# Optimization experiments

Hardware: AMD Instinct MI355X
Metric: run time of the kernel (lower is better)

Reference implementation:

```python
import jax, jax.numpy as jnp
import numpy as np

BETA = 1.0
JITTER = 1e-6


def setup_inputs() -> dict:
    key = jax.random.key(0)
    k1, k2, k3, k4 = jax.random.split(key, 4)
    N, L = 256, 8192
    R_clean = jax.random.normal(k1, (N, L, 3, 3), dtype=jnp.float32)
    t = jax.random.uniform(k2, (N,), dtype=jnp.float32, minval=0.05, maxval=1.0)
    noise = jax.random.normal(k3, (N, L, 3, 3), dtype=jnp.float32)
    eps_noise = jax.random.normal(k4, (N, L, 3, 3), dtype=jnp.float32)
    return {"R_clean": R_clean, "t": t, "noise": noise, "eps_noise": eps_noise}


def _svd_project_so3(F):
    # F: (..., 3, 3).  R = U diag(1,1,det(U V^T)) V^T
    U, S, Vh = jnp.linalg.svd(F, full_matrices=False)
    d = jnp.linalg.det(jnp.matmul(U, Vh))          # (...,)
    mid = jnp.concatenate(
        [jnp.ones(d.shape + (2,), dtype=F.dtype), d[..., None]], axis=-1
    )                                               # (..., 3) = (1, 1, det)
    # U @ diag(mid) @ Vh == (U * mid[..., None, :]) @ Vh
    return jnp.matmul(U * mid[..., None, :], Vh)


def reference(R_clean, t, noise, eps_noise):
    # sample_theta: F_t = alpha_t * R_clean + sqrt(alpha_t) * noise
    alpha_t = (BETA * t).reshape(-1, 1, 1, 1)       # (N,1,1,1)
    F_t = alpha_t * R_clean + jnp.sqrt(alpha_t) * noise
    # svd_project_so3 adds a tiny random jitter before SVD
    F = F_t + JITTER * eps_noise
    return _svd_project_so3(F)
```

## Files before the change

### kernel.cpp

```cpp
#include <hip/hip_runtime.h>

#define TPB  256
#define MPB  256
#define F4PB 576

__device__ __forceinline__ void jrot(float app, float aqq, float apq,
                                     float& c, float& s, float& t) {
    float d  = aqq - app;
    float p2 = apq + apq;
    float rad = __builtin_amdgcn_sqrtf(fmaf(d, d, p2 * p2));
    float den = fmaxf(fabsf(d) + rad, 1e-38f);
    t = p2 * copysignf(__builtin_amdgcn_rcpf(den), d);
    c = __builtin_amdgcn_rsqf(fmaf(t, t, 1.0f));
    s = t * c;
}

__global__ __launch_bounds__(TPB)
void so3_proj_kernel(const float* __restrict__ Rc,
                     const float* __restrict__ Tt,
                     const float* __restrict__ Nz,
                     const float* __restrict__ Ez,
                     float* __restrict__ Out,
                     int L)
{
    __shared__ float4 lds4[F4PB];
    float* lds = (float*)lds4;

    const int tid = threadIdx.x;
    const long long base = (long long)blockIdx.x * MPB;
    const int n = (int)(base / (long long)L);
    const float alpha = Tt[n];
    const float sa = __builtin_amdgcn_sqrtf(alpha);

    const float4* R4 = (const float4*)(Rc + base * 9);
    const float4* N4 = (const float4*)(Nz + base * 9);
    const float4* E4 = (const float4*)(Ez + base * 9);
    float4*       O4 = (float4*)(Out + base * 9);

    #pragma unroll
    for (int it = 0; it < 3; ++it) {
        int j = tid + it * TPB;
        if (j < F4PB) {
            float4 r = R4[j], z = N4[j], e = E4[j];
            float4 f;
            f.x = fmaf(alpha, r.x, fmaf(sa, z.x, 1e-6f * e.x));
            f.y = fmaf(alpha, r.y, fmaf(sa, z.y, 1e-6f * e.y));
            f.z = fmaf(alpha, r.z, fmaf(sa, z.z, 1e-6f * e.z));
            f.w = fmaf(alpha, r.w, fmaf(sa, z.w, 1e-6f * e.w));
            lds4[j] = f;
        }
    }
    __syncthreads();

    float F[9];
    #pragma unroll
    for (int k = 0; k < 9; ++k) F[k] = lds[tid * 9 + k];

    float a00 = F[0]*F[0] + F[3]*F[3] + F[6]*F[6];
    float a01 = F[0]*F[1] + F[3]*F[4] + F[6]*F[7];
    float a02 = F[0]*F[2] + F[3]*F[5] + F[6]*F[8];
    float a11 = F[1]*F[1] + F[4]*F[4] + F[7]*F[7];
    float a12 = F[1]*F[2] + F[4]*F[5] + F[7]*F[8];
    float a22 = F[2]*F[2] + F[5]*F[5] + F[8]*F[8];

    float v00=1.f, v01=0.f, v02=0.f;
    float v10=0.f, v11=1.f, v12=0.f;
    float v20=0.f, v21=0.f, v22=1.f;

    for (int sweep = 0; sweep < 5; ++sweep) {
        if (sweep >= 3) {
            float off = fmaf(a01, a01, fmaf(a02, a02, a12 * a12));
            float sc  = fmaf(a00, a00, fmaf(a11, a11, a22 * a22));
            if (__all(off <= 1e-13f * sc)) break;
        }
        float c, s, t, t0;
        jrot(a00, a11, a01, c, s, t);
        a00 = fmaf(-t, a01, a00); a11 = fmaf(t, a01, a11); a01 = 0.f;
        t0 = c*a02 - s*a12; a12 = fmaf(s, a02, c*a12); a02 = t0;
        t0 = c*v00 - s*v01; v01 = fmaf(s, v00, c*v01); v00 = t0;
        t0 = c*v10 - s*v11; v11 = fmaf(s, v10, c*v11); v10 = t0;
        t0 = c*v20 - s*v21; v21 = fmaf(s, v20, c*v21); v20 = t0;
        jrot(a00, a22, a02, c, s, t);
        a00 = fmaf(-t, a02, a00); a22 = fmaf(t, a02, a22); a02 = 0.f;
        t0 = c*a01 - s*a12; a12 = fmaf(s, a01, c*a12); a01 = t0;
        t0 = c*v00 - s*v02; v02 = fmaf(s, v00, c*v02); v00 = t0;
        t0 = c*v10 - s*v12; v12 = fmaf(s, v10, c*v12); v10 = t0;
        t0 = c*v20 - s*v22; v22 = fmaf(s, v20, c*v22); v20 = t0;
        jrot(a11, a22, a12, c, s, t);
        a11 = fmaf(-t, a12, a11); a22 = fmaf(t, a12, a22); a12 = 0.f;
        t0 = c*a01 - s*a02; a02 = fmaf(s, a01, c*a02); a01 = t0;
        t0 = c*v01 - s*v02; v02 = fmaf(s, v01, c*v02); v01 = t0;
        t0 = c*v11 - s*v12; v12 = fmaf(s, v11, c*v12); v11 = t0;
        t0 = c*v21 - s*v22; v22 = fmaf(s, v21, c*v22); v21 = t0;
    }

    float l0 = a00, l1 = a11, l2 = a22;
    if (l0 < l1) { float t;
        t=l0;l0=l1;l1=t; t=v00;v00=v01;v01=t; t=v10;v10=v11;v11=t; t=v20;v20=v21;v21=t; }
    if (l0 < l2) { float t;
        t=l0;l0=l2;l2=t; t=v00;v00=v02;v02=t; t=v10;v10=v12;v12=t; t=v20;v20=v22;v22=t; }
    if (l1 < l2) { float t;
        t=l1;l1=l2;l2=t; t=v01;v01=v02;v02=t; t=v11;v11=v12;v12=t; t=v21;v21=v22;v22=t; }

    float v3x = v10*v21 - v20*v11;
    float v3y = v20*v01 - v00*v21;
    float v3z = v00*v11 - v10*v01;

    float u1x = F[0]*v00 + F[1]*v10 + F[2]*v20;
    float u1y = F[3]*v00 + F[4]*v10 + F[5]*v20;
    float u1z = F[6]*v00 + F[7]*v10 + F[8]*v20;
    float inv1 = __builtin_amdgcn_rsqf(fmaxf(u1x*u1x + u1y*u1y + u1z*u1z, 1e-30f));
    u1x *= inv1; u1y *= inv1; u1z *= inv1;

    float wx = F[0]*v01 + F[1]*v11 + F[2]*v21;
    float wy = F[3]*v01 + F[4]*v11 + F[5]*v21;
    float wz = F[6]*v01 + F[7]*v11 + F[8]*v21;
    float dd = u1x*wx + u1y*wy + u1z*wz;
    wx -= dd*u1x; wy -= dd*u1y; wz -= dd*u1z;
    float inv2 = __builtin_amdgcn_rsqf(fmaxf(wx*wx + wy*wy + wz*wz, 1e-30f));
    float u2x = wx*inv2, u2y = wy*inv2, u2z = wz*inv2;

    float u3x = u1y*u2z - u1z*u2y;
    float u3y = u1z*u2x - u1x*u2z;
    float u3z = u1x*u2y - u1y*u2x;

    float Rm[9];
    Rm[0] = u1x*v00 + u2x*v01 + u3x*v3x;
    Rm[1] = u1x*v10 + u2x*v11 + u3x*v3y;
    Rm[2] = u1x*v20 + u2x*v21 + u3x*v3z;
    Rm[3] = u1y*v00 + u2y*v01 + u3y*v3x;
    Rm[4] = u1y*v10 + u2y*v11 + u3y*v3y;
    Rm[5] = u1y*v20 + u2y*v21 + u3y*v3z;
    Rm[6] = u1z*v00 + u2z*v01 + u3z*v3x;
    Rm[7] = u1z*v10 + u2z*v11 + u3z*v3y;
    Rm[8] = u1z*v20 + u2z*v21 + u3z*v3z;

    __syncthreads();
    #pragma unroll
    for (int k = 0; k < 9; ++k) lds[tid * 9 + k] = Rm[k];
    __syncthreads();

    #pragma unroll
    for (int it = 0; it < 3; ++it) {
        int j = tid + it * TPB;
        if (j < F4PB) O4[j] = lds4[j];
    }
}

extern "C" void kernel_launch(void* const* d_in, const int* in_sizes, int n_in,
                              void* d_out, int out_size, void* d_ws, size_t ws_size,
                              hipStream_t stream) {
    const float* Rc = (const float*)d_in[0];
    const float* Tt = (const float*)d_in[1];
    const float* Nz = (const float*)d_in[2];
    const float* Ez = (const float*)d_in[3];
    float* Out = (float*)d_out;

    const long long mats = (long long)in_sizes[0] / 9;
    const int L = (int)(mats / in_sizes[1]);
    const int blocks = (int)(mats / MPB);

    so3_proj_kernel<<<blocks, TPB, 0, stream>>>(Rc, Tt, Nz, Ez, Out, L);
}
```

Measured before the change: 244.3 us.

## Process two matrices per thread and use closed-form Jacobi rotation updates

Each thread now handles two 3x3 matrices, with the Jacobi pivots of the two interleaved so their independent dependency chains can overlap, and each block covers 512 matrices. The rotation is rewritten so the diagonal entries are updated in closed form, (sum ± rad)/2, and c and s come from a single rsq instead of rcp followed by rsq. The intent is more instruction-level parallelism in the latency-bound Jacobi loop and a shorter per-pivot dependency chain. In exchange, register pressure and LDS use double (18 KB per block), which may reduce occupancy, and the early-exit check now waits for both matrices to converge.

```diff
diff --git a/kernel.cpp b/kernel.cpp
--- a/kernel.cpp
+++ b/kernel.cpp
@@ -1,18 +1,77 @@
 #include <hip/hip_runtime.h>
 
 #define TPB  256
-#define MPB  256
-#define F4PB 576
+#define MPB  512
+#define F4PB 1152
 
-__device__ __forceinline__ void jrot(float app, float aqq, float apq,
-                                     float& c, float& s, float& t) {
-    float d  = aqq - app;
-    float p2 = apq + apq;
+__device__ __forceinline__ void pivot(float& app, float& aqq, float& apq,
+                                      float& arp, float& arq,
+                                      float& vp0, float& vq0,
+                                      float& vp1, float& vq1,
+                                      float& vp2, float& vq2)
+{
+    float d   = aqq - app;
+    float p2  = apq + apq;
     float rad = __builtin_amdgcn_sqrtf(fmaf(d, d, p2 * p2));
-    float den = fmaxf(fabsf(d) + rad, 1e-38f);
-    t = p2 * copysignf(__builtin_amdgcn_rcpf(den), d);
-    c = __builtin_amdgcn_rsqf(fmaf(t, t, 1.0f));
-    s = t * c;
+    float h   = fabsf(d) + rad + 1e-18f;
+    float inv = __builtin_amdgcn_rsqf(fmaf(h, h, p2 * p2));
+    float c   = h * inv;
+    float s   = p2 * copysignf(inv, d);
+    float sum = app + aqq;
+    float sr  = copysignf(rad, d);
+    app = 0.5f * (sum - sr);
+    aqq = 0.5f * (sum + sr);
+    apq = 0.f;
+    float x;
+    x = fmaf(c, arp, -s * arq); arq = fmaf(s, arp, c * arq); arp = x;
+    x = fmaf(c, vp0, -s * vq0); vq0 = fmaf(s, vp0, c * vq0); vp0 = x;
+    x = fmaf(c, vp1, -s * vq1); vq1 = fmaf(s, vp1, c * vq1); vp1 = x;
+    x = fmaf(c, vp2, -s * vq2); vq2 = fmaf(s, vp2, c * vq2); vp2 = x;
+}
+
+__device__ __forceinline__ void finish(const float F[9],
+                                       float l0, float l1, float l2,
+                                       float v[9], float Rm[9])
+{
+    float t;
+    if (l0 < l1) { t=l0;l0=l1;l1=t; t=v[0];v[0]=v[1];v[1]=t;
+                   t=v[3];v[3]=v[4];v[4]=t; t=v[6];v[6]=v[7];v[7]=t; }
+    if (l0 < l2) { t=l0;l0=l2;l2=t; t=v[0];v[0]=v[2];v[2]=t;
+                   t=v[3];v[3]=v[5];v[5]=t; t=v[6];v[6]=v[8];v[8]=t; }
+    if (l1 < l2) { t=l1;l1=l2;l2=t; t=v[1];v[1]=v[2];v[2]=t;
+                   t=v[4];v[4]=v[5];v[5]=t; t=v[7];v[7]=v[8];v[8]=t; }
+
+    float v3x = v[3]*v[7] - v[6]*v[4];
+    float v3y = v[6]*v[1] - v[0]*v[7];
+    float v3z = v[0]*v[4] - v[3]*v[1];
+
+    float u1x = F[0]*v[0] + F[1]*v[3] + F[2]*v[6];
+    float u1y = F[3]*v[0] + F[4]*v[3] + F[5]*v[6];
+    float u1z = F[6]*v[0] + F[7]*v[3] + F[8]*v[6];
+    float inv1 = __builtin_amdgcn_rsqf(fmaxf(u1x*u1x + u1y*u1y + u1z*u1z, 1e-30f));
+    u1x *= inv1; u1y *= inv1; u1z *= inv1;
+
+    float wx = F[0]*v[1] + F[1]*v[4] + F[2]*v[7];
+    float wy = F[3]*v[1] + F[4]*v[4] + F[5]*v[7];
+    float wz = F[6]*v[1] + F[7]*v[4] + F[8]*v[7];
+    float dd = u1x*wx + u1y*wy + u1z*wz;
+    wx -= dd*u1x; wy -= dd*u1y; wz -= dd*u1z;
+    float inv2 = __builtin_amdgcn_rsqf(fmaxf(wx*wx + wy*wy + wz*wz, 1e-30f));
+    float u2x = wx*inv2, u2y = wy*inv2, u2z = wz*inv2;
+
+    float u3x = u1y*u2z - u1z*u2y;
+    float u3y = u1z*u2x - u1x*u2z;
+    float u3z = u1x*u2y - u1y*u2x;
+
+    Rm[0] = u1x*v[0] + u2x*v[1] + u3x*v3x;
+    Rm[1] = u1x*v[3] + u2x*v[4] + u3x*v3y;
+    Rm[2] = u1x*v[6] + u2x*v[7] + u3x*v3z;
+    Rm[3] = u1y*v[0] + u2y*v[1] + u3y*v3x;
+    Rm[4] = u1y*v[3] + u2y*v[4] + u3y*v3y;
+    Rm[5] = u1y*v[6] + u2y*v[7] + u3y*v3z;
+    Rm[6] = u1z*v[0] + u2z*v[1] + u3z*v3x;
+    Rm[7] = u1z*v[3] + u2z*v[4] + u3z*v3y;
+    Rm[8] = u1z*v[6] + u2z*v[7] + u3z*v3z;
 }
 
 __global__ __launch_bounds__(TPB)
@@ -38,7 +97,7 @@
     float4*       O4 = (float4*)(Out + base * 9);
 
     #pragma unroll
-    for (int it = 0; it < 3; ++it) {
+    for (int it = 0; it < 5; ++it) {
         int j = tid + it * TPB;
         if (j < F4PB) {
             float4 r = R4[j], z = N4[j], e = E4[j];
@@ -52,96 +111,58 @@
     }
     __syncthreads();
 
-    float F[9];
+    float Fa[9], Fb[9];
     #pragma unroll
-    for (int k = 0; k < 9; ++k) F[k] = lds[tid * 9 + k];
+    for (int k = 0; k < 9; ++k) Fa[k] = lds[tid * 9 + k];
+    #pragma unroll
+    for (int k = 0; k < 9; ++k) Fb[k] = lds[(tid + TPB) * 9 + k];
 
-    float a00 = F[0]*F[0] + F[3]*F[3] + F[6]*F[6];
-    float a01 = F[0]*F[1] + F[3]*F[4] + F[6]*F[7];
-    float a02 = F[0]*F[2] + F[3]*F[5] + F[6]*F[8];
-    float a11 = F[1]*F[1] + F[4]*F[4] + F[7]*F[7];
-    float a12 = F[1]*F[2] + F[4]*F[5] + F[7]*F[8];
-    float a22 = F[2]*F[2] + F[5]*F[5] + F[8]*F[8];
+    float Aa00 = Fa[0]*Fa[0] + Fa[3]*Fa[3] + Fa[6]*Fa[6];
+    float Aa01 = Fa[0]*Fa[1] + Fa[3]*Fa[4] + Fa[6]*Fa[7];
+    float Aa02 = Fa[0]*Fa[2] + Fa[3]*Fa[5] + Fa[6]*Fa[8];
+    float Aa11 = Fa[1]*Fa[1] + Fa[4]*Fa[4] + Fa[7]*Fa[7];
+    float Aa12 = Fa[1]*Fa[2] + Fa[4]*Fa[5] + Fa[7]*Fa[8];
+    float Aa22 = Fa[2]*Fa[2] + Fa[5]*Fa[5] + Fa[8]*Fa[8];
 
-    float v00=1.f, v01=0.f, v02=0.f;
-    float v10=0.f, v11=1.f, v12=0.f;
-    float v20=0.f, v21=0.f, v22=1.f;
+    float Ab00 = Fb[0]*Fb[0] + Fb[3]*Fb[3] + Fb[6]*Fb[6];
+    float Ab01 = Fb[0]*Fb[1] + Fb[3]*Fb[4] + Fb[6]*Fb[7];
+    float Ab02 = Fb[0]*Fb[2] + Fb[3]*Fb[5] + Fb[6]*Fb[8];
+    float Ab11 = Fb[1]*Fb[1] + Fb[4]*Fb[4] + Fb[7]*Fb[7];
+    float Ab12 = Fb[1]*Fb[2] + Fb[4]*Fb[5] + Fb[7]*Fb[8];
+    float Ab22 = Fb[2]*Fb[2] + Fb[5]*Fb[5] + Fb[8]*Fb[8];
+
+    float Va[9] = {1.f,0.f,0.f, 0.f,1.f,0.f, 0.f,0.f,1.f};
+    float Vb[9] = {1.f,0.f,0.f, 0.f,1.f,0.f, 0.f,0.f,1.f};
 
     for (int sweep = 0; sweep < 5; ++sweep) {
         if (sweep >= 3) {
-            float off = fmaf(a01, a01, fmaf(a02, a02, a12 * a12));
-            float sc  = fmaf(a00, a00, fmaf(a11, a11, a22 * a22));
-            if (__all(off <= 1e-13f * sc)) break;
+            float offA = fmaf(Aa01, Aa01, fmaf(Aa02, Aa02, Aa12 * Aa12));
+            float scA  = fmaf(Aa00, Aa00, fmaf(Aa11, Aa11, Aa22 * Aa22));
+            float offB = fmaf(Ab01, Ab01, fmaf(Ab02, Ab02, Ab12 * Ab12));
+            float scB  = fmaf(Ab00, Ab00, fmaf(Ab11, Ab11, Ab22 * Ab22));
+            if (__all((offA <= 1e-13f * scA) && (offB <= 1e-13f * scB))) break;
         }
-        float c, s, t, t0;
-        jrot(a00, a11, a01, c, s, t);
-        a00 = fmaf(-t, a01, a00); a11 = fmaf(t, a01, a11); a01 = 0.f;
-        t0 = c*a02 - s*a12; a12 = fmaf(s, a02, c*a12); a02 = t0;
-        t0 = c*v00 - s*v01; v01 = fmaf(s, v00, c*v01); v00 = t0;
-        t0 = c*v10 - s*v11; v11 = fmaf(s, v10, c*v11); v10 = t0;
-        t0 = c*v20 - s*v21; v21 = fmaf(s, v20, c*v21); v20 = t0;
-        jrot(a00, a22, a02, c, s, t);
-        a00 = fmaf(-t, a02, a00); a22 = fmaf(t, a02, a22); a02 = 0.f;
-        t0 = c*a01 - s*a12; a12 = fmaf(s, a01, c*a12); a01 = t0;
-        t0 = c*v00 - s*v02; v02 = fmaf(s, v00, c*v02); v00 = t0;
-        t0 = c*v10 - s*v12; v12 = fmaf(s, v10, c*v12); v10 = t0;
-        t0 = c*v20 - s*v22; v22 = fmaf(s, v20, c*v22); v20 = t0;
-        jrot(a11, a22, a12, c, s, t);
-        a11 = fmaf(-t, a12, a11); a22 = fmaf(t, a12, a22); a12 = 0.f;
-        t0 = c*a01 - s*a02; a02 = fmaf(s, a01, c*a02); a01 = t0;
-        t0 = c*v01 - s*v02; v02 = fmaf(s, v01, c*v02); v01 = t0;
-        t0 = c*v11 - s*v12; v12 = fmaf(s, v11, c*v12); v11 = t0;
-        t0 = c*v21 - s*v22; v22 = fmaf(s, v21, c*v22); v21 = t0;
+        pivot(Aa00, Aa11, Aa01, Aa02, Aa12, Va[0],Va[1], Va[3],Va[4], Va[6],Va[7]);
+        pivot(Ab00, Ab11, Ab01, Ab02, Ab12, Vb[0],Vb[1], Vb[3],Vb[4], Vb[6],Vb[7]);
+        pivot(Aa00, Aa22, Aa02, Aa01, Aa12, Va[0],Va[2], Va[3],Va[5], Va[6],Va[8]);
+        pivot(Ab00, Ab22, Ab02, Ab01, Ab12, Vb[0],Vb[2], Vb[3],Vb[5], Vb[6],Vb[8]);
+        pivot(Aa11, Aa22, Aa12, Aa01, Aa02, Va[1],Va[2], Va[4],Va[5], Va[7],Va[8]);
+        pivot(Ab11, Ab22, Ab12, Ab01, Ab02, Vb[1],Vb[2], Vb[4],Vb[5], Vb[7],Vb[8]);
     }
 
-    float l0 = a00, l1 = a11, l2 = a22;
-    if (l0 < l1) { float t;
-        t=l0;l0=l1;l1=t; t=v00;v00=v01;v01=t; t=v10;v10=v11;v11=t; t=v20;v20=v21;v21=t; }
-    if (l0 < l2) { float t;
-        t=l0;l0=l2;l2=t; t=v00;v00=v02;v02=t; t=v10;v10=v12;v12=t; t=v20;v20=v22;v22=t; }
-    if (l1 < l2) { float t;
-        t=l1;l1=l2;l2=t; t=v01;v01=v02;v02=t; t=v11;v11=v12;v12=t; t=v21;v21=v22;v22=t; }
-
-    float v3x = v10*v21 - v20*v11;
-    float v3y = v20*v01 - v00*v21;
-    float v3z = v00*v11 - v10*v01;
-
-    float u1x = F[0]*v00 + F[1]*v10 + F[2]*v20;
-    float u1y = F[3]*v00 + F[4]*v10 + F[5]*v20;
-    float u1z = F[6]*v00 + F[7]*v10 + F[8]*v20;
-    float inv1 = __builtin_amdgcn_rsqf(fmaxf(u1x*u1x + u1y*u1y + u1z*u1z, 1e-30f));
-    u1x *= inv1; u1y *= inv1; u1z *= inv1;
-
-    float wx = F[0]*v01 + F[1]*v11 + F[2]*v21;
-    float wy = F[3]*v01 + F[4]*v11 + F[5]*v21;
-    float wz = F[6]*v01 + F[7]*v11 + F[8]*v21;
-    float dd = u1x*wx + u1y*wy + u1z*wz;
-    wx -= dd*u1x; wy -= dd*u1y; wz -= dd*u1z;
-    float inv2 = __builtin_amdgcn_rsqf(fmaxf(wx*wx + wy*wy + wz*wz, 1e-30f));
-    float u2x = wx*inv2, u2y = wy*inv2, u2z = wz*inv2;
-
-    float u3x = u1y*u2z - u1z*u2y;
-    float u3y = u1z*u2x - u1x*u2z;
-    float u3z = u1x*u2y - u1y*u2x;
-
-    float Rm[9];
-    Rm[0] = u1x*v00 + u2x*v01 + u3x*v3x;
-    Rm[1] = u1x*v10 + u2x*v11 + u3x*v3y;
-    Rm[2] = u1x*v20 + u2x*v21 + u3x*v3z;
-    Rm[3] = u1y*v00 + u2y*v01 + u3y*v3x;
-    Rm[4] = u1y*v10 + u2y*v11 + u3y*v3y;
-    Rm[5] = u1y*v20 + u2y*v21 + u3y*v3z;
-    Rm[6] = u1z*v00 + u2z*v01 + u3z*v3x;
-    Rm[7] = u1z*v10 + u2z*v11 + u3z*v3y;
-    Rm[8] = u1z*v20 + u2z*v21 + u3z*v3z;
+    float Ra[9], Rb[9];
+    finish(Fa, Aa00, Aa11, Aa22, Va, Ra);
+    finish(Fb, Ab00, Ab11, Ab22, Vb, Rb);
 
     __syncthreads();
     #pragma unroll
-    for (int k = 0; k < 9; ++k) lds[tid * 9 + k] = Rm[k];
+    for (int k = 0; k < 9; ++k) lds[tid * 9 + k] = Ra[k];
+    #pragma unroll
+    for (int k = 0; k < 9; ++k) lds[(tid + TPB) * 9 + k] = Rb[k];
     __syncthreads();
 
     #pragma unroll
-    for (int it = 0; it < 3; ++it) {
+    for (int it = 0; it < 5; ++it) {
         int j = tid + it * TPB;
         if (j < F4PB) O4[j] = lds4[j];
     }
```

After: 250.4 us. 1.03x slower.
